# Kernel tuning notes

Measured on AMD Instinct MI355X. Metric: run time of the kernel, lower is better.

## Reference

```python
import jax, jax.numpy as jnp
import numpy as np

EPS = 1e-8
LAM = 20.0  # lambda_softmax
I, R, T, W, D = 128, 48, 64, 100, 768


def l2norm(x, axis=-1):
    # matches torch l2norm: x / (sqrt(sum(x^2)) + eps)
    return x / (jnp.sqrt(jnp.sum(x * x, axis=axis, keepdims=True)) + EPS)


def _safe_div(num, den):
    return num / jnp.where(den > 0, den, 1.0)


def setup_inputs() -> dict:
    key = jax.random.key(0)
    k1, k2, k3, k4, k5 = jax.random.split(key, 5)
    return {
        "local_img_query": jax.random.normal(k1, (I, R, D), jnp.float32),
        "local_img_value": jax.random.normal(k2, (I, R, D), jnp.float32),
        "local_text_key": jax.random.normal(k3, (T, W, D), jnp.float32),
        "local_text_value": jax.random.normal(k4, (T, W, D), jnp.float32),
        "text_length": jax.random.randint(k5, (T,), 8, W + 1),
    }


def reference(local_img_query, local_img_value, local_text_key, local_text_value, text_length):
    # Vectorized over texts: padding words are masked instead of sliced,
    # reproducing the per-text ragged loop of compute_weiTexts exactly.
    Tn, Wn, Dn = local_text_key.shape
    In, Rn, _ = local_img_query.shape
    dtype = local_img_query.dtype
    mask = jnp.arange(Wn)[None, :] < text_length[:, None]          # [T,W] valid words
    Lf = text_length.astype(dtype)

    imgQn = l2norm(local_img_query)                                 # [I,R,D]
    txtKn = l2norm(local_text_key)                                  # [T,W,D]
    # cosine scores, shared by both directions (t2i uses the transpose)
    sim = jnp.einsum('twd,ird->tiwr', txtKn, imgQn)                 # [T,I,W,R]
    a = jax.nn.leaky_relu(sim, 0.1)

    # ---- i2t: query = image regions, source = text words ----
    ai = l2norm(a, axis=-1)                                         # l2norm over R per word row
    ai = jnp.swapaxes(ai, 2, 3)                                     # [T,I,R,W]
    m4 = mask[:, None, None, :]
    attn = jax.nn.softmax(jnp.where(m4, ai * LAM, -1e30), axis=-1)  # softmax over valid words
    attn = attn * m4
    # focal_equal with true source length L_i
    funcF = attn * Lf[:, None, None, None] - jnp.sum(attn, -1, keepdims=True)
    tmp = jnp.where(funcF > 0, attn, 0.0)
    attn = _safe_div(tmp, jnp.sum(tmp, -1, keepdims=True))
    weiText = l2norm(jnp.einsum('tirw,twd->tird', attn, local_text_value))  # [T,I,R,D]
    num = jnp.sum(local_img_value[None] * weiText, -1)
    den = jnp.maximum(jnp.linalg.norm(local_img_value, axis=-1)[None]
                      * jnp.linalg.norm(weiText, axis=-1), EPS)
    i2t = jnp.mean(num / den, axis=-1)                              # [T,I]

    # ---- t2i: query = text words, source = image regions ----
    a2 = jnp.swapaxes(a, 2, 3) * m4                                 # [T,I,R,W]; zero padded words before l2norm over W
    a2 = l2norm(a2, axis=-1)
    a2 = jnp.swapaxes(a2, 2, 3)                                     # [T,I,W,R]
    attn2 = jax.nn.softmax(a2 * LAM, axis=-1)                       # softmax over regions (dense)
    funcF2 = attn2 * Rn - jnp.sum(attn2, -1, keepdims=True)
    tmp2 = jnp.where(funcF2 > 0, attn2, 0.0)
    attn2 = _safe_div(tmp2, jnp.sum(tmp2, -1, keepdims=True))
    weiImage = l2norm(jnp.einsum('tiwr,ird->tiwd', attn2, local_img_value))  # [T,I,W,D]
    num2 = jnp.sum(local_text_value[:, None] * weiImage, -1)        # [T,I,W]
    den2 = jnp.maximum(jnp.linalg.norm(local_text_value, axis=-1)[:, None]
                       * jnp.linalg.norm(weiImage, axis=-1), EPS)
    sim2 = jnp.where(mask[:, None, :], num2 / den2, 0.0)
    t2i = jnp.sum(sim2, axis=-1) / Lf[:, None]                      # masked mean over valid words, [T,I]

    return i2t.T, t2i.T                                             # ([n_img,n_txt], [n_img,n_txt])
```

## Files before the change

### kernel.cpp

```cpp
#include <hip/hip_runtime.h>

#define EPS   1e-8f
#define LAMB  20.0f
#define NI    128
#define NR    48
#define NT    64
#define NW    100
#define ND    768

typedef unsigned int uint;
typedef unsigned short ushortt;
typedef __attribute__((ext_vector_type(8))) short short8;
typedef __attribute__((ext_vector_type(4))) float f32x4;

#define OFF_KHI  102400ULL
#define OFF_KLO  11112448ULL
#define OFF_QHI  22122496ULL
#define OFF_QLO  31559680ULL
#define OFF_TVB  40996864ULL
#define OFF_IVB  52006912ULL
#define OFF_MH   61444096ULL
#define OFF_ML   63279104ULL
#define OFF_HH   65114112ULL
#define OFF_HL   65900544ULL
#define WS_NEED  66686976ULL

__device__ inline unsigned short f2bf(float f) {
    uint u = __float_as_uint(f);
    u = (u + 0x7fffu + ((u >> 16) & 1u)) >> 16;
    return (unsigned short)u;
}
__device__ inline float bf2f(unsigned short h) {
    return __uint_as_float((uint)h << 16);
}
__device__ inline void split_store(float4 v, ushortt* hp, ushortt* lp) {
    unsigned short h0 = f2bf(v.x), h1 = f2bf(v.y), h2 = f2bf(v.z), h3 = f2bf(v.w);
    float f0 = bf2f(h0), f1 = bf2f(h1), f2 = bf2f(h2), f3 = bf2f(h3);
    ushort4 H; H.x = h0; H.y = h1; H.z = h2; H.w = h3;
    ushort4 L2; L2.x = f2bf(v.x - f0); L2.y = f2bf(v.y - f1); L2.z = f2bf(v.z - f2); L2.w = f2bf(v.w - f3);
    *(ushort4*)hp = H;
    *(ushort4*)lp = L2;
}
__device__ inline int swzATT(int r, int w) {
    return r * 128 + ((((w >> 3) ^ (r & 7)) << 3) | (w & 7));
}
__device__ inline int swzATT2(int w, int r) {
    return w * 64 + ((((r >> 3) ^ (w & 7)) << 3) | (r & 7));
}
__device__ inline float wredsum(float v) {
#pragma unroll
    for (int m = 1; m < 64; m <<= 1) v += __shfl_xor(v, m, 64);
    return v;
}
__device__ inline float wredmax(float v) {
#pragma unroll
    for (int m = 1; m < 64; m <<= 1) v = fmaxf(v, __shfl_xor(v, m, 64));
    return v;
}

__global__ void nafs_norms(const float* __restrict__ imgQ,
                           const float* __restrict__ imgV,
                           const float* __restrict__ txtK,
                           const float* __restrict__ txtV,
                           float* __restrict__ ws) {
    int row  = blockIdx.x * 4 + (threadIdx.x >> 6);
    int lane = threadIdx.x & 63;
    const float* src;
    int inv;
    if (row < 6144)       { src = imgQ + (size_t)row * ND;           inv = 1; }
    else if (row < 12544) { src = txtK + (size_t)(row - 6144) * ND;  inv = 1; }
    else if (row < 18688) { src = imgV + (size_t)(row - 12544) * ND; inv = 0; }
    else                  { src = txtV + (size_t)(row - 18688) * ND; inv = 0; }
    float ss = 0.f;
#pragma unroll
    for (int j = 0; j < 3; ++j) {
        float4 v = *(const float4*)(src + j * 256 + lane * 4);
        ss += v.x * v.x + v.y * v.y + v.z * v.z + v.w * v.w;
    }
#pragma unroll
    for (int off = 32; off > 0; off >>= 1) ss += __shfl_down(ss, off, 64);
    if (lane == 0) {
        float n = sqrtf(ss);
        ws[row] = inv ? (1.0f / (n + EPS)) : n;
    }
}

__global__ void nafs_convert(const float* __restrict__ txtK,
                             const float* __restrict__ imgQ,
                             const float* __restrict__ txtV,
                             const float* __restrict__ imgV,
                             const float* __restrict__ ws,
                             ushortt* __restrict__ khi, ushortt* __restrict__ klo,
                             ushortt* __restrict__ qhi, ushortt* __restrict__ qlo,
                             ushortt* __restrict__ tvb, ushortt* __restrict__ ivb) {
    int row = blockIdx.x;
    int c4  = threadIdx.x;
    const int dc32 = c4 >> 3;
    const int quad = (c4 & 7) >> 1;
    const int j0   = (c4 & 1) * 4;
    if (row < 7168) {
        int t = row / 112, w = row % 112;
        int m = w >> 4, l15 = w & 15;
        size_t o = ((size_t)(t * 7 + m) * 24 + dc32) * 512 + (quad * 16 + l15) * 8 + j0;
        if (w < NW) {
            float s = ws[6144 + t * NW + w];
            float4 v = *(const float4*)&txtK[((size_t)t * NW + w) * ND + c4 * 4];
            v.x *= s; v.y *= s; v.z *= s; v.w *= s;
            split_store(v, &khi[o], &klo[o]);
        } else {
            ushort4 z; z.x = z.y = z.z = z.w = 0;
            *(ushort4*)&khi[o] = z; *(ushort4*)&klo[o] = z;
        }
    } else if (row < 13312) {
        int q = row - 7168;
        int ii = q / 48, r = q % 48;
        int n = r >> 4, l15 = r & 15;
        float s = ws[q];
        float4 v = *(const float4*)&imgQ[(size_t)q * ND + c4 * 4];
        v.x *= s; v.y *= s; v.z *= s; v.w *= s;
        size_t o = ((size_t)(ii * 3 + n) * 24 + dc32) * 512 + (quad * 16 + l15) * 8 + j0;
        split_store(v, &qhi[o], &qlo[o]);
    } else if (row < 20480) {
        int rr = row - 13312;
        int t = rr / 112, w = rr % 112;
        int m = w >> 4, l15 = w & 15;
        size_t o = ((size_t)(t * 7 + m) * 24 + dc32) * 512 + (quad * 16 + l15) * 8 + j0;
        ushort4 u; u.x = u.y = u.z = u.w = 0;
        if (w < NW) {
            float4 v = *(const float4*)&txtV[((size_t)t * NW + w) * ND + c4 * 4];
            u.x = f2bf(v.x); u.y = f2bf(v.y); u.z = f2bf(v.z); u.w = f2bf(v.w);
        }
        *(ushort4*)&tvb[o] = u;
    } else {
        int rr = row - 20480;
        int ii = rr / 48, r = rr % 48;
        int n = r >> 4, l15 = r & 15;
        size_t o = ((size_t)(ii * 3 + n) * 24 + dc32) * 512 + (quad * 16 + l15) * 8 + j0;
        float4 v = *(const float4*)&imgV[(size_t)rr * ND + c4 * 4];
        ushort4 u; u.x = f2bf(v.x); u.y = f2bf(v.y); u.z = f2bf(v.z); u.w = f2bf(v.w);
        *(ushort4*)&ivb[o] = u;
    }
}

__global__ void nafs_gram_m(const ushortt* __restrict__ tvb,
                            ushortt* __restrict__ mh, ushortt* __restrict__ ml) {
    const int t = blockIdx.x;
    const int tid = threadIdx.x, wv = tid >> 6, lane = tid & 63;
    const int quad = lane >> 4, l15 = lane & 15;
    const ushortt* base = tvb + (size_t)t * 7 * 24 * 512;
    ushortt* mhB = mh + (size_t)t * 7 * 4 * 512;
    ushortt* mlB = ml + (size_t)t * 7 * 4 * 512;
#pragma unroll
    for (int a = 0; a < 2; ++a) {
        int m = wv + 4 * a;
        if (m < 7) {
            f32x4 c[7];
#pragma unroll
            for (int n = 0; n < 7; ++n) c[n] = (f32x4){0.f, 0.f, 0.f, 0.f};
            for (int dc32 = 0; dc32 < 24; ++dc32) {
                short8 av = *(const short8*)&base[((size_t)m * 24 + dc32) * 512 + lane * 8];
#pragma unroll
                for (int n = 0; n < 7; ++n) {
                    short8 bv = *(const short8*)&base[((size_t)n * 24 + dc32) * 512 + lane * 8];
                    c[n] = __builtin_amdgcn_mfma_f32_16x16x32_bf16(av, bv, c[n], 0, 0, 0);
                }
            }
#pragma unroll
            for (int n = 0; n < 7; ++n)
#pragma unroll
                for (int reg = 0; reg < 4; ++reg) {
                    int wc = n * 16 + l15;
                    int lrow = quad * 4 + reg;
                    float v = c[n][reg];
                    ushortt h = f2bf(v);
                    size_t fo = ((size_t)m * 4 + (wc >> 5)) * 512
                              + ((((wc >> 3) & 3) * 16 + lrow) * 8) + (wc & 7);
                    mhB[fo] = h;
                    mlB[fo] = f2bf(v - bf2f(h));
                }
        }
    }
    for (int idx = tid; idx < 7 * 32; idx += 256) {
        int m = idx >> 5, ln = 32 + (idx & 31);
        short8 z = (short8){0, 0, 0, 0, 0, 0, 0, 0};
        size_t fo = ((size_t)m * 4 + 3) * 512 + (size_t)ln * 8;
        *(short8*)&mhB[fo] = z; *(short8*)&mlB[fo] = z;
    }
}

__global__ void nafs_gram_h(const ushortt* __restrict__ ivb,
                            ushortt* __restrict__ hh, ushortt* __restrict__ hl) {
    const int i = blockIdx.x;
    const int tid = threadIdx.x, wv = tid >> 6, lane = tid & 63;
    const int quad = lane >> 4, l15 = lane & 15;
    const ushortt* base = ivb + (size_t)i * 3 * 24 * 512;
    ushortt* hhB = hh + (size_t)i * 3 * 2 * 512;
    ushortt* hlB = hl + (size_t)i * 3 * 2 * 512;
    if (wv < 3) {
        int m = wv;
        f32x4 c[3];
#pragma unroll
        for (int n = 0; n < 3; ++n) c[n] = (f32x4){0.f, 0.f, 0.f, 0.f};
        for (int dc32 = 0; dc32 < 24; ++dc32) {
            short8 av = *(const short8*)&base[((size_t)m * 24 + dc32) * 512 + lane * 8];
#pragma unroll
            for (int n = 0; n < 3; ++n) {
                short8 bv = *(const short8*)&base[((size_t)n * 24 + dc32) * 512 + lane * 8];
                c[n] = __builtin_amdgcn_mfma_f32_16x16x32_bf16(av, bv, c[n], 0, 0, 0);
            }
        }
#pragma unroll
        for (int n = 0; n < 3; ++n)
#pragma unroll
            for (int reg = 0; reg < 4; ++reg) {
                int rc = n * 16 + l15;
                int lrow = quad * 4 + reg;
                float v = c[n][reg];
                ushortt h = f2bf(v);
                size_t fo = ((size_t)m * 2 + (rc >> 5)) * 512
                          + ((((rc >> 3) & 3) * 16 + lrow) * 8) + (rc & 7);
                hhB[fo] = h;
                hlB[fo] = f2bf(v - bf2f(h));
            }
    }
    for (int idx = tid; idx < 3 * 32; idx += 256) {
        int m = idx >> 5, ln = 32 + (idx & 31);
        short8 z = (short8){0, 0, 0, 0, 0, 0, 0, 0};
        size_t fo = ((size_t)m * 2 + 1) * 512 + (size_t)ln * 8;
        *(short8*)&hhB[fo] = z; *(short8*)&hlB[fo] = z;
    }
}

__global__ __launch_bounds__(256, 2)
void nafs_fused3(const int*  __restrict__ tlen,
                 const float* __restrict__ ws,
                 const ushortt* __restrict__ khi, const ushortt* __restrict__ klo,
                 const ushortt* __restrict__ qhi, const ushortt* __restrict__ qlo,
                 const ushortt* __restrict__ tvb, const ushortt* __restrict__ ivb,
                 const ushortt* __restrict__ mh, const ushortt* __restrict__ ml,
                 const ushortt* __restrict__ hh, const ushortt* __restrict__ hl,
                 float* __restrict__ out) {
    __shared__ __align__(16) ushortt shATT[48 * 128];
    __shared__ __align__(16) ushortt shATT2[112 * 64];
    __shared__ float sCol[NR], sSe1[NR], sS11[NR], sS21[NR];
    __shared__ float sCos1[NR], sCos2[112];
    __shared__ float sSS1[NR], sDD1[NR], sSS2[112], sDD2[112];

    const int tid  = threadIdx.x;
    const int wv   = tid >> 6;
    const int lane = tid & 63;
    const int quad = lane >> 4;
    const int l15  = lane & 15;
    const int key  = l15 & 7;
    const int b    = blockIdx.x;
    const int xcd  = b & 7;
    const int idx  = b >> 3;
    const int st   = idx >> 6;
    const int rem  = idx & 63;
    const int i    = (xcd << 4) | (rem >> 2);
    const int t    = (st << 2) | (rem & 3);
    const int L    = tlen[t];
    const float Lf = (float)L;

    const float* __restrict__ nVi = ws + 12544;
    const float* __restrict__ nVt = ws + 18688;

    if (tid < NR) {
        sSS1[tid] = 0.f; sDD1[tid] = 0.f;
        sCol[tid] = 0.f; sSe1[tid] = 0.f; sS11[tid] = 0.f; sS21[tid] = 0.f;
    }
    for (int idx2 = tid; idx2 < 112 * 2; idx2 += 256) {
        int w = idx2 >> 1, nb = 6 + (idx2 & 1);
        short8 z = (short8){0, 0, 0, 0, 0, 0, 0, 0};
        *(short8*)&shATT2[w * 64 + ((nb ^ (w & 7)) << 3)] = z;
    }
    __syncthreads();

    const int m0  = wv, m1 = wv + 4;
    const int m1c = (m1 == 7) ? 6 : m1;
    const size_t kb0 = ((size_t)(t * 7 + m0)) * 24 * 512 + (size_t)lane * 8;
    const size_t kb1 = ((size_t)(t * 7 + m1c)) * 24 * 512 + (size_t)lane * 8;
    const size_t qb  = ((size_t)(i * 3)) * 24 * 512 + (size_t)lane * 8;
    const ushortt* fK0h = khi + kb0;
    const ushortt* fK0l = klo + kb0;
    const ushortt* fK1h = khi + kb1;
    const ushortt* fK1l = klo + kb1;
    const ushortt* fQh  = qhi + qb;
    const ushortt* fQl  = qlo + qb;
    const ushortt* fA0  = tvb + kb0;
    const ushortt* fA1  = tvb + kb1;
    const ushortt* fB   = ivb + qb;

    f32x4 acc[2][3];
    f32x4 gf[2][3];
#pragma unroll
    for (int a = 0; a < 2; ++a)
#pragma unroll
        for (int n = 0; n < 3; ++n) {
            acc[a][n] = (f32x4){0.f, 0.f, 0.f, 0.f};
            gf[a][n]  = (f32x4){0.f, 0.f, 0.f, 0.f};
        }

    for (int dc32 = 0; dc32 < 24; ++dc32) {
        const int o = dc32 * 512;
        short8 a0h = *(const short8*)(fK0h + o);
        short8 a0l = *(const short8*)(fK0l + o);
        short8 a1h = *(const short8*)(fK1h + o);
        short8 a1l = *(const short8*)(fK1l + o);
        short8 b0h = *(const short8*)(fQh + o);
        short8 b0l = *(const short8*)(fQl + o);
        short8 b1h = *(const short8*)(fQh + 12288 + o);
        short8 b1l = *(const short8*)(fQl + 12288 + o);
        short8 b2h = *(const short8*)(fQh + 24576 + o);
        short8 b2l = *(const short8*)(fQl + 24576 + o);
        short8 tA0 = *(const short8*)(fA0 + o);
        short8 tA1 = *(const short8*)(fA1 + o);
        short8 tB0 = *(const short8*)(fB + o);
        short8 tB1 = *(const short8*)(fB + 12288 + o);
        short8 tB2 = *(const short8*)(fB + 24576 + o);

        acc[0][0] = __builtin_amdgcn_mfma_f32_16x16x32_bf16(a0h, b0h, acc[0][0], 0, 0, 0);
        acc[0][0] = __builtin_amdgcn_mfma_f32_16x16x32_bf16(a0h, b0l, acc[0][0], 0, 0, 0);
        acc[0][0] = __builtin_amdgcn_mfma_f32_16x16x32_bf16(a0l, b0h, acc[0][0], 0, 0, 0);
        acc[0][1] = __builtin_amdgcn_mfma_f32_16x16x32_bf16(a0h, b1h, acc[0][1], 0, 0, 0);
        acc[0][1] = __builtin_amdgcn_mfma_f32_16x16x32_bf16(a0h, b1l, acc[0][1], 0, 0, 0);
        acc[0][1] = __builtin_amdgcn_mfma_f32_16x16x32_bf16(a0l, b1h, acc[0][1], 0, 0, 0);
        acc[0][2] = __builtin_amdgcn_mfma_f32_16x16x32_bf16(a0h, b2h, acc[0][2], 0, 0, 0);
        acc[0][2] = __builtin_amdgcn_mfma_f32_16x16x32_bf16(a0h, b2l, acc[0][2], 0, 0, 0);
        acc[0][2] = __builtin_amdgcn_mfma_f32_16x16x32_bf16(a0l, b2h, acc[0][2], 0, 0, 0);
        acc[1][0] = __builtin_amdgcn_mfma_f32_16x16x32_bf16(a1h, b0h, acc[1][0], 0, 0, 0);
        acc[1][0] = __builtin_amdgcn_mfma_f32_16x16x32_bf16(a1h, b0l, acc[1][0], 0, 0, 0);
        acc[1][0] = __builtin_amdgcn_mfma_f32_16x16x32_bf16(a1l, b0h, acc[1][0], 0, 0, 0);
        acc[1][1] = __builtin_amdgcn_mfma_f32_16x16x32_bf16(a1h, b1h, acc[1][1], 0, 0, 0);
        acc[1][1] = __builtin_amdgcn_mfma_f32_16x16x32_bf16(a1h, b1l, acc[1][1], 0, 0, 0);
        acc[1][1] = __builtin_amdgcn_mfma_f32_16x16x32_bf16(a1l, b1h, acc[1][1], 0, 0, 0);
        acc[1][2] = __builtin_amdgcn_mfma_f32_16x16x32_bf16(a1h, b2h, acc[1][2], 0, 0, 0);
        acc[1][2] = __builtin_amdgcn_mfma_f32_16x16x32_bf16(a1h, b2l, acc[1][2], 0, 0, 0);
        acc[1][2] = __builtin_amdgcn_mfma_f32_16x16x32_bf16(a1l, b2h, acc[1][2], 0, 0, 0);

        gf[0][0] = __builtin_amdgcn_mfma_f32_16x16x32_bf16(tA0, tB0, gf[0][0], 0, 0, 0);
        gf[0][1] = __builtin_amdgcn_mfma_f32_16x16x32_bf16(tA0, tB1, gf[0][1], 0, 0, 0);
        gf[0][2] = __builtin_amdgcn_mfma_f32_16x16x32_bf16(tA0, tB2, gf[0][2], 0, 0, 0);
        gf[1][0] = __builtin_amdgcn_mfma_f32_16x16x32_bf16(tA1, tB0, gf[1][0], 0, 0, 0);
        gf[1][1] = __builtin_amdgcn_mfma_f32_16x16x32_bf16(tA1, tB1, gf[1][1], 0, 0, 0);
        gf[1][2] = __builtin_amdgcn_mfma_f32_16x16x32_bf16(tA1, tB2, gf[1][2], 0, 0, 0);
    }

    float lk[2][3][4];
#pragma unroll
    for (int a = 0; a < 2; ++a) {
        int m = wv + 4 * a;
        bool ok = (m < 7);
#pragma unroll
        for (int n = 0; n < 3; ++n)
#pragma unroll
            for (int reg = 0; reg < 4; ++reg) {
                float s = ok ? acc[a][n][reg] : 0.f;
                lk[a][n][reg] = (s > 0.f) ? s : 0.1f * s;
            }
    }

    float invW[2][4];
#pragma unroll
    for (int a = 0; a < 2; ++a)
#pragma unroll
        for (int reg = 0; reg < 4; ++reg) {
            float ss = 0.f;
#pragma unroll
            for (int n = 0; n < 3; ++n) ss = fmaf(lk[a][n][reg], lk[a][n][reg], ss);
            ss += __shfl_xor(ss, 1, 64); ss += __shfl_xor(ss, 2, 64);
            ss += __shfl_xor(ss, 4, 64); ss += __shfl_xor(ss, 8, 64);
            invW[a][reg] = 1.0f / (sqrtf(ss) + EPS);
        }

    float e1[2][3][4];
    {
        float cs[3] = {0.f, 0.f, 0.f}, es[3] = {0.f, 0.f, 0.f};
#pragma unroll
        for (int a = 0; a < 2; ++a) {
            int m = wv + 4 * a;
#pragma unroll
            for (int reg = 0; reg < 4; ++reg) {
                int w = m * 16 + quad * 4 + reg;
                bool act = (m < 7) && (w < L);
#pragma unroll
                for (int n = 0; n < 3; ++n) {
                    float v = lk[a][n][reg];
                    float e = act ? __expf(v * invW[a][reg] * LAMB) : 0.f;
                    e1[a][n][reg] = e;
                    if (act) cs[n] = fmaf(v, v, cs[n]);
                    es[n] += e;
                }
            }
        }
#pragma unroll
        for (int n = 0; n < 3; ++n) {
            float c = cs[n], e = es[n];
            c += __shfl_xor(c, 16, 64); c += __shfl_xor(c, 32, 64);
            e += __shfl_xor(e, 16, 64); e += __shfl_xor(e, 32, 64);
            if (quad == 0) {
                atomicAdd(&sCol[n * 16 + l15], c);
                atomicAdd(&sSe1[n * 16 + l15], e);
            }
        }
    }
    __syncthreads();

    {
        float inv2[3];
#pragma unroll
        for (int n = 0; n < 3; ++n) inv2[n] = 1.0f / (sqrtf(sCol[n * 16 + l15]) + EPS);
#pragma unroll
        for (int a = 0; a < 2; ++a) {
            int m = wv + 4 * a;
            if (m < 7) {
#pragma unroll
                for (int reg = 0; reg < 4; ++reg) {
                    int w = m * 16 + quad * 4 + reg;
                    float e2[3];
                    float se = 0.f;
#pragma unroll
                    for (int n = 0; n < 3; ++n) {
                        float e = __expf(lk[a][n][reg] * inv2[n] * LAMB);
                        e2[n] = e; se += e;
                    }
                    se += __shfl_xor(se, 1, 64); se += __shfl_xor(se, 2, 64);
                    se += __shfl_xor(se, 4, 64); se += __shfl_xor(se, 8, 64);
                    float inv = 1.0f / se;
                    float S1 = e2[0] * inv + e2[1] * inv + e2[2] * inv;
                    S1 += __shfl_xor(S1, 1, 64); S1 += __shfl_xor(S1, 2, 64);
                    S1 += __shfl_xor(S1, 4, 64); S1 += __shfl_xor(S1, 8, 64);
                    float sel[3];
                    float S2 = 0.f;
#pragma unroll
                    for (int n = 0; n < 3; ++n) {
                        float p = e2[n] * inv;
                        sel[n] = ((p * 48.0f - S1) > 0.f) ? p : 0.f;
                        S2 += sel[n];
                    }
                    S2 += __shfl_xor(S2, 1, 64); S2 += __shfl_xor(S2, 2, 64);
                    S2 += __shfl_xor(S2, 4, 64); S2 += __shfl_xor(S2, 8, 64);
                    float iS2 = 1.0f / ((S2 > 0.f) ? S2 : 1.0f);
                    bool rowOK = (w < L);
#pragma unroll
                    for (int n = 0; n < 3; ++n) {
                        float val = rowOK ? sel[n] * iS2 : 0.f;
                        shATT2[swzATT2(w, n * 16 + l15)] = f2bf(val);
                    }
                }
            }
        }
    }

    float invSe[3];
#pragma unroll
    for (int n = 0; n < 3; ++n) invSe[n] = 1.0f / sSe1[n * 16 + l15];
    {
        float s1p[3] = {0.f, 0.f, 0.f};
#pragma unroll
        for (int a = 0; a < 2; ++a)
#pragma unroll
            for (int n = 0; n < 3; ++n)
#pragma unroll
                for (int reg = 0; reg < 4; ++reg)
                    s1p[n] += e1[a][n][reg] * invSe[n];
#pragma unroll
        for (int n = 0; n < 3; ++n) {
            float v = s1p[n];
            v += __shfl_xor(v, 16, 64); v += __shfl_xor(v, 32, 64);
            if (quad == 0) atomicAdd(&sS11[n * 16 + l15], v);
        }
    }
    __syncthreads();

    {
        float s2p[3] = {0.f, 0.f, 0.f};
#pragma unroll
        for (int n = 0; n < 3; ++n) {
            float S1r = sS11[n * 16 + l15];
#pragma unroll
            for (int a = 0; a < 2; ++a)
#pragma unroll
                for (int reg = 0; reg < 4; ++reg) {
                    float p = e1[a][n][reg] * invSe[n];
                    s2p[n] += ((p * Lf - S1r) > 0.f) ? p : 0.f;
                }
        }
#pragma unroll
        for (int n = 0; n < 3; ++n) {
            float v = s2p[n];
            v += __shfl_xor(v, 16, 64); v += __shfl_xor(v, 32, 64);
            if (quad == 0) atomicAdd(&sS21[n * 16 + l15], v);
        }
    }
    __syncthreads();

    {
#pragma unroll
        for (int n = 0; n < 3; ++n) {
            int r = n * 16 + l15;
            float S1r = sS11[r];
            float s2  = sS21[r];
            float iS2 = 1.0f / ((s2 > 0.f) ? s2 : 1.0f);
#pragma unroll
            for (int a = 0; a < 2; ++a) {
                int m = wv + 4 * a;
                ushortt v4[4];
#pragma unroll
                for (int reg = 0; reg < 4; ++reg) {
                    float p  = e1[a][n][reg] * invSe[n];
                    float tm = ((p * Lf - S1r) > 0.f) ? p : 0.f;
                    v4[reg] = f2bf(tm * iS2);
                }
                int wb = m * 16 + quad * 4;
                int f  = (((wb >> 3) ^ (r & 7)) << 3) | (wb & 7);
                *(ushort4*)&shATT[r * 128 + f] = *(ushort4*)v4;
            }
        }
    }
    __syncthreads();

    {
        float pd1[3] = {0.f, 0.f, 0.f};
#pragma unroll
        for (int a = 0; a < 2; ++a) {
            int m = wv + 4 * a;
            if (m < 7) {
#pragma unroll
                for (int reg = 0; reg < 4; ++reg) {
                    int w = m * 16 + quad * 4 + reg;
                    float p2 = 0.f;
#pragma unroll
                    for (int n = 0; n < 3; ++n) {
                        int r = n * 16 + l15;
                        float gv = gf[a][n][reg];
                        p2 = fmaf(gv, bf2f(shATT2[swzATT2(w, r)]), p2);
                        pd1[n] = fmaf(gv, bf2f(shATT[swzATT(r, w)]), pd1[n]);
                    }
                    p2 += __shfl_xor(p2, 1, 64); p2 += __shfl_xor(p2, 2, 64);
                    p2 += __shfl_xor(p2, 4, 64); p2 += __shfl_xor(p2, 8, 64);
                    if (l15 == 0) sDD2[w] = p2;
                }
            }
        }
#pragma unroll
        for (int n = 0; n < 3; ++n) {
            float p = pd1[n];
            p += __shfl_xor(p, 16, 64); p += __shfl_xor(p, 32, 64);
            if (quad == 0) atomicAdd(&sDD1[n * 16 + l15], p);
        }
    }

    {
        short8 af[3][4];
#pragma unroll
        for (int mt = 0; mt < 3; ++mt)
#pragma unroll
            for (int ks = 0; ks < 4; ++ks)
                af[mt][ks] = *(const short8*)&shATT[(mt * 16 + l15) * 128 + (((ks * 4 + quad) ^ key) << 3)];
        float ps[3][4];
#pragma unroll
        for (int mt = 0; mt < 3; ++mt)
#pragma unroll
            for (int reg = 0; reg < 4; ++reg) ps[mt][reg] = 0.f;
#pragma unroll
        for (int p = 0; p < 2; ++p) {
            int nt = wv + 4 * p;
            if (nt < 7) {
                const ushortt* pMh = mh + ((size_t)(t * 7 + nt)) * 4 * 512 + (size_t)lane * 8;
                const ushortt* pMl = ml + ((size_t)(t * 7 + nt)) * 4 * 512 + (size_t)lane * 8;
                short8 bh[4], bl[4];
#pragma unroll
                for (int ks = 0; ks < 4; ++ks) {
                    bh[ks] = *(const short8*)(pMh + ks * 512);
                    bl[ks] = *(const short8*)(pMl + ks * 512);
                }
                f32x4 y[3];
#pragma unroll
                for (int mt = 0; mt < 3; ++mt) y[mt] = (f32x4){0.f, 0.f, 0.f, 0.f};
#pragma unroll
                for (int mt = 0; mt < 3; ++mt)
#pragma unroll
                    for (int ks = 0; ks < 4; ++ks) {
                        y[mt] = __builtin_amdgcn_mfma_f32_16x16x32_bf16(af[mt][ks], bh[ks], y[mt], 0, 0, 0);
                        y[mt] = __builtin_amdgcn_mfma_f32_16x16x32_bf16(af[mt][ks], bl[ks], y[mt], 0, 0, 0);
                    }
                int wc = nt * 16 + l15;
#pragma unroll
                for (int mt = 0; mt < 3; ++mt)
#pragma unroll
                    for (int reg = 0; reg < 4; ++reg) {
                        int r = mt * 16 + quad * 4 + reg;
                        ps[mt][reg] = fmaf(y[mt][reg], bf2f(shATT[swzATT(r, wc)]), ps[mt][reg]);
                    }
            }
        }
#pragma unroll
        for (int mt = 0; mt < 3; ++mt)
#pragma unroll
            for (int reg = 0; reg < 4; ++reg) {
                float p = ps[mt][reg];
                p += __shfl_xor(p, 1, 64); p += __shfl_xor(p, 2, 64);
                p += __shfl_xor(p, 4, 64); p += __shfl_xor(p, 8, 64);
                if (l15 == 0) atomicAdd(&sSS1[mt * 16 + quad * 4 + reg], p);
            }
    }

    {
        short8 zbh[3][2], zbl[3][2];
#pragma unroll
        for (int n = 0; n < 3; ++n) {
#pragma unroll
            for (int ks = 0; ks < 2; ++ks) {
                size_t fo = (((size_t)(i * 3 + n)) * 2 + ks) * 512 + (size_t)lane * 8;
                zbh[n][ks] = *(const short8*)&hh[fo];
                zbl[n][ks] = *(const short8*)&hl[fo];
            }
        }
#pragma unroll
        for (int a = 0; a < 2; ++a) {
            int m = wv + 4 * a;
            if (m < 7) {
                f32x4 z[3];
#pragma unroll
                for (int n = 0; n < 3; ++n) z[n] = (f32x4){0.f, 0.f, 0.f, 0.f};
#pragma unroll
                for (int ks = 0; ks < 2; ++ks) {
                    short8 a2f = *(const short8*)&shATT2[(m * 16 + l15) * 64 + (((ks * 4 + quad) ^ key) << 3)];
#pragma unroll
                    for (int n = 0; n < 3; ++n) {
                        z[n] = __builtin_amdgcn_mfma_f32_16x16x32_bf16(a2f, zbh[n][ks], z[n], 0, 0, 0);
                        z[n] = __builtin_amdgcn_mfma_f32_16x16x32_bf16(a2f, zbl[n][ks], z[n], 0, 0, 0);
                    }
                }
#pragma unroll
                for (int reg = 0; reg < 4; ++reg) {
                    int w = m * 16 + quad * 4 + reg;
                    float p = 0.f;
#pragma unroll
                    for (int n = 0; n < 3; ++n)
                        p = fmaf(z[n][reg], bf2f(shATT2[swzATT2(w, n * 16 + l15)]), p);
                    p += __shfl_xor(p, 1, 64); p += __shfl_xor(p, 2, 64);
                    p += __shfl_xor(p, 4, 64); p += __shfl_xor(p, 8, 64);
                    if (l15 == 0) sSS2[w] = p;
                }
            }
        }
    }
    __syncthreads();

    if (tid < NR) {
        float s = fmaxf(sSS1[tid], 0.f), d = sDD1[tid];
        float nu  = sqrtf(s);
        float num = d / (nu + EPS);
        float den = fmaxf(nVi[i * NR + tid] * (nu / (nu + EPS)), EPS);
        sCos1[tid] = num / den;
    } else if (tid >= 64 && tid < 176) {
        int w = tid - 64;
        if (w < L) {
            float s = fmaxf(sSS2[w], 0.f), d = sDD2[w];
            float nu  = sqrtf(s);
            float num = d / (nu + EPS);
            float den = fmaxf(nVt[t * NW + w] * (nu / (nu + EPS)), EPS);
            sCos2[w] = num / den;
        }
    }
    __syncthreads();
    if (tid == 0) {
        float s = 0.f;
        for (int r = 0; r < NR; ++r) s += sCos1[r];
        out[i * NT + t] = s * (1.0f / 48.0f);
    } else if (tid == 64) {
        float s = 0.f;
        for (int w = 0; w < L; ++w) s += sCos2[w];
        out[NI * NT + i * NT + t] = s / Lf;
    }
}

#define A_KH   0
#define A_KL   4480
#define A_QH   8960
#define A_QL   10880
#define A_ATT  0
#define A_ATT2 6528
#define SHA_SZ 14592
#define B1_TVT 3200
#define B2_IVT 6656
#define SHB_SZ 4900

__global__ __launch_bounds__(256, 3)
void nafs_fused_fb(const float* __restrict__ imgQ,
                   const float* __restrict__ imgV,
                   const float* __restrict__ txtK,
                   const float* __restrict__ txtV,
                   const int*  __restrict__ tlen,
                   const float* __restrict__ ws,
                   float* __restrict__ out) {
    __shared__ ushortt shA[SHA_SZ];
    __shared__ float shB[SHB_SZ];
    __shared__ float sKs[NW], sQs[NR], sInvW[NW], sInv2[NR], sCos1[NR], sCos2[112];

    const int tid  = threadIdx.x;
    const int wv   = tid >> 6;
    const int lane = tid & 63;
    const int quad = lane >> 4;
    const int l15  = lane & 15;
    const int b    = blockIdx.x;
    const int t    = b >> 7;
    const int i    = b & 127;
    const int L    = tlen[t];
    const float Lf = (float)L;

    const float* __restrict__ invQ = ws;
    const float* __restrict__ invK = ws + 6144;
    const float* __restrict__ nVi  = ws + 12544;
    const float* __restrict__ nVt  = ws + 18688;

    const float* Kbase  = txtK + (size_t)t * (NW * ND);
    const float* Qbase  = imgQ + (size_t)i * (NR * ND);
    const float* TVbase = txtV + (size_t)t * (NW * ND);
    const float* IVbase = imgV + (size_t)i * (NR * ND);

    if (tid < NW)                  sKs[tid]       = invK[t * NW + tid];
    else if (tid < NW + NR)        sQs[tid - NW]  = invQ[i * NR + (tid - NW)];

    const int mt0 = wv * 2, mt1 = wv * 2 + 1;
    f32x4 acc[2][3];
#pragma unroll
    for (int a = 0; a < 2; ++a)
#pragma unroll
        for (int n = 0; n < 3; ++n) acc[a][n] = (f32x4){0.f, 0.f, 0.f, 0.f};

    for (int dc = 0; dc < ND; dc += 32) {
        __syncthreads();
        for (int idx = tid; idx < 112 * 8; idx += 256) {
            int w = idx >> 3, seg = idx & 7;
            float4 v;
            if (w < NW) {
                v = *(const float4*)(Kbase + (size_t)w * ND + dc + seg * 4);
                float s = sKs[w];
                v.x *= s; v.y *= s; v.z *= s; v.w *= s;
            } else { v.x = v.y = v.z = v.w = 0.f; }
            split_store(v, &shA[A_KH + w * 40 + seg * 4], &shA[A_KL + w * 40 + seg * 4]);
        }
        for (int idx = tid; idx < NR * 8; idx += 256) {
            int r = idx >> 3, seg = idx & 7;
            float4 v = *(const float4*)(Qbase + (size_t)r * ND + dc + seg * 4);
            float s = sQs[r];
            v.x *= s; v.y *= s; v.z *= s; v.w *= s;
            split_store(v, &shA[A_QH + r * 40 + seg * 4], &shA[A_QL + r * 40 + seg * 4]);
        }
        __syncthreads();
        short8 bh[3], bl[3];
#pragma unroll
        for (int n = 0; n < 3; ++n) {
            bh[n] = *(const short8*)&shA[A_QH + (n * 16 + l15) * 40 + quad * 8];
            bl[n] = *(const short8*)&shA[A_QL + (n * 16 + l15) * 40 + quad * 8];
        }
#pragma unroll
        for (int a = 0; a < 2; ++a) {
            int m = (a == 0) ? mt0 : mt1;
            if (m < 7) {
                short8 ah = *(const short8*)&shA[A_KH + (m * 16 + l15) * 40 + quad * 8];
                short8 al = *(const short8*)&shA[A_KL + (m * 16 + l15) * 40 + quad * 8];
#pragma unroll
                for (int n = 0; n < 3; ++n) {
                    acc[a][n] = __builtin_amdgcn_mfma_f32_16x16x32_bf16(ah, bh[n], acc[a][n], 0, 0, 0);
                    acc[a][n] = __builtin_amdgcn_mfma_f32_16x16x32_bf16(ah, bl[n], acc[a][n], 0, 0, 0);
                    acc[a][n] = __builtin_amdgcn_mfma_f32_16x16x32_bf16(al, bh[n], acc[a][n], 0, 0, 0);
                }
            }
        }
    }
    __syncthreads();
#pragma unroll
    for (int a = 0; a < 2; ++a) {
        int m = (a == 0) ? mt0 : mt1;
        if (m < 7) {
#pragma unroll
            for (int n = 0; n < 3; ++n)
#pragma unroll
                for (int reg = 0; reg < 4; ++reg) {
                    int w = m * 16 + quad * 4 + reg;
                    if (w < NW) {
                        float s = acc[a][n][reg];
                        shB[w * 49 + n * 16 + l15] = (s > 0.f) ? s : 0.1f * s;
                    }
                }
        }
    }
    __syncthreads();

    if (tid < NW) {
        float ssum = 0.f;
#pragma unroll 8
        for (int r = 0; r < NR; ++r) { float v = shB[tid * 49 + r]; ssum += v * v; }
        sInvW[tid] = 1.0f / (sqrtf(ssum) + EPS);
    } else if (tid >= 128 && tid < 128 + NR) {
        int r = tid - 128;
        float ssum = 0.f;
        for (int w = 0; w < L; ++w) { float v = shB[w * 49 + r]; ssum += v * v; }
        sInv2[r] = 1.0f / (sqrtf(ssum) + EPS);
    }
    __syncthreads();

    for (int r = wv; r < NR; r += 4) {
        int w1 = lane, w2 = lane + 64;
        int v1ok = (w1 < L), v2ok = (w2 < L);
        float v1 = v1ok ? shB[w1 * 49 + r] * sInvW[w1] * LAMB : -1e30f;
        float v2 = v2ok ? shB[w2 * 49 + r] * sInvW[w2] * LAMB : -1e30f;
        float m  = wredmax(fmaxf(v1, v2));
        float e1 = v1ok ? expf(v1 - m) : 0.f;
        float e2 = v2ok ? expf(v2 - m) : 0.f;
        float inv = 1.0f / wredsum(e1 + e2);
        float p1 = e1 * inv, p2 = e2 * inv;
        float S1 = wredsum(p1 + p2);
        float t1 = ((p1 * Lf - S1) > 0.f) ? p1 : 0.f;
        float t2 = ((p2 * Lf - S1) > 0.f) ? p2 : 0.f;
        float S2 = wredsum(t1 + t2);
        float iS2 = 1.0f / ((S2 > 0.f) ? S2 : 1.0f);
        shA[A_ATT + r * 136 + w1] = f2bf(t1 * iS2);
        shA[A_ATT + r * 136 + w2] = f2bf(t2 * iS2);
    }
    for (int w = wv; w < L; w += 4) {
        int rok = (lane < NR);
        float v = rok ? shB[w * 49 + lane] * sInv2[lane] * LAMB : -1e30f;
        float m = wredmax(v);
        float e = rok ? expf(v - m) : 0.f;
        float inv = 1.0f / wredsum(e);
        float p = e * inv;
        float S1 = wredsum(p);
        float tm = ((p * 48.0f - S1) > 0.f) ? p : 0.f;
        float S2 = wredsum(tm);
        float iS2 = 1.0f / ((S2 > 0.f) ? S2 : 1.0f);
        shA[A_ATT2 + w * 72 + lane] = f2bf(tm * iS2);
    }
    for (int w = L + wv; w < 112; w += 4) shA[A_ATT2 + w * 72 + lane] = 0;
    __syncthreads();

    ushortt* shBu = (ushortt*)shB;
    const int kk = (L + 31) >> 5;
    float ss1[4] = {0.f, 0.f, 0.f, 0.f}, dd1[4] = {0.f, 0.f, 0.f, 0.f};
    const int mt = wv;
    const int cgrp = tid >> 5, ccol = tid & 31;

    for (int cc = 0; cc < ND; cc += 32) {
        __syncthreads();
        for (int w = cgrp; w < 128; w += 8) {
            float val = (w < NW) ? TVbase[(size_t)w * ND + cc + ccol] : 0.f;
            shBu[B1_TVT + ccol * 136 + w] = f2bf(val);
        }
        for (int idx = tid; idx < NR * 8; idx += 256) {
            int r = idx >> 3, seg = idx & 7;
            float4 v = *(const float4*)(IVbase + (size_t)r * ND + cc + seg * 4);
            float* p = &shB[r * 33 + seg * 4];
            p[0] = v.x; p[1] = v.y; p[2] = v.z; p[3] = v.w;
        }
        __syncthreads();
        if (mt < 3) {
            f32x4 u[2] = {(f32x4){0.f,0.f,0.f,0.f}, (f32x4){0.f,0.f,0.f,0.f}};
            for (int ks = 0; ks < kk; ++ks) {
                short8 a = *(const short8*)&shA[A_ATT + (mt * 16 + l15) * 136 + ks * 32 + quad * 8];
#pragma unroll
                for (int n = 0; n < 2; ++n) {
                    short8 bb = *(const short8*)&shBu[B1_TVT + (n * 16 + l15) * 136 + ks * 32 + quad * 8];
                    u[n] = __builtin_amdgcn_mfma_f32_16x16x32_bf16(a, bb, u[n], 0, 0, 0);
                }
            }
#pragma unroll
            for (int n = 0; n < 2; ++n)
#pragma unroll
                for (int reg = 0; reg < 4; ++reg) {
                    int r = mt * 16 + quad * 4 + reg;
                    float uu = u[n][reg];
                    ss1[reg] = fmaf(uu, uu, ss1[reg]);
                    dd1[reg] = fmaf(uu, shB[r * 33 + n * 16 + l15], dd1[reg]);
                }
        }
    }
    if (mt < 3) {
#pragma unroll
        for (int reg = 0; reg < 4; ++reg) {
            float s = ss1[reg], d = dd1[reg];
#pragma unroll
            for (int m = 1; m < 16; m <<= 1) { s += __shfl_xor(s, m, 64); d += __shfl_xor(d, m, 64); }
            if (l15 == 0) {
                int r = mt * 16 + quad * 4 + reg;
                float nu  = sqrtf(s);
                float num = d / (nu + EPS);
                float den = fmaxf(nVi[i * NR + r] * (nu / (nu + EPS)), EPS);
                sCos1[r] = num / den;
            }
        }
    }

    const int ntot = (L + 15) >> 4;
    float ss2[2] = {0.f, 0.f}, dd2[2] = {0.f, 0.f};

    for (int cc = 0; cc < ND; cc += 32) {
        __syncthreads();
        for (int idx = tid; idx < NW * 8; idx += 256) {
            int w = idx >> 3, seg = idx & 7;
            float4 v = *(const float4*)(TVbase + (size_t)w * ND + cc + seg * 4);
            float* p = &shB[w * 33 + seg * 4];
            p[0] = v.x; p[1] = v.y; p[2] = v.z; p[3] = v.w;
        }
        for (int r = cgrp; r < 64; r += 8) {
            float val = (r < NR) ? IVbase[(size_t)r * ND + cc + ccol] : 0.f;
            shBu[B2_IVT + ccol * 72 + r] = f2bf(val);
        }
        __syncthreads();
#pragma unroll
        for (int pp = 0; pp < 2; ++pp) {
            int nt = wv + 4 * pp;
            if (nt < ntot) {
                f32x4 u[2] = {(f32x4){0.f,0.f,0.f,0.f}, (f32x4){0.f,0.f,0.f,0.f}};
#pragma unroll
                for (int ks = 0; ks < 2; ++ks) {
                    short8 bb = *(const short8*)&shA[A_ATT2 + (nt * 16 + l15) * 72 + ks * 32 + quad * 8];
#pragma unroll
                    for (int mm = 0; mm < 2; ++mm) {
                        short8 aa = *(const short8*)&shBu[B2_IVT + (mm * 16 + l15) * 72 + ks * 32 + quad * 8];
                        u[mm] = __builtin_amdgcn_mfma_f32_16x16x32_bf16(aa, bb, u[mm], 0, 0, 0);
                    }
                }
                int w = nt * 16 + l15;
                float tvok = (w < L) ? 1.f : 0.f;
#pragma unroll
                for (int mm = 0; mm < 2; ++mm)
#pragma unroll
                    for (int reg = 0; reg < 4; ++reg) {
                        int c = mm * 16 + quad * 4 + reg;
                        float uu = u[mm][reg];
                        float tv = (w < L) ? shB[w * 33 + c] : 0.f;
                        ss2[pp] = fmaf(uu, uu, ss2[pp]);
                        dd2[pp] = fmaf(uu, tv * tvok, dd2[pp]);
                    }
            }
        }
    }
#pragma unroll
    for (int pp = 0; pp < 2; ++pp) {
        int nt = wv + 4 * pp;
        if (nt < ntot) {
            float s = ss2[pp], d = dd2[pp];
            s += __shfl_xor(s, 16, 64); d += __shfl_xor(d, 16, 64);
            s += __shfl_xor(s, 32, 64); d += __shfl_xor(d, 32, 64);
            if (quad == 0) {
                int w = nt * 16 + l15;
                if (w < L) {
                    float nu  = sqrtf(s);
                    float num = d / (nu + EPS);
                    float den = fmaxf(nVt[t * NW + w] * (nu / (nu + EPS)), EPS);
                    sCos2[w] = num / den;
                }
            }
        }
    }
    __syncthreads();
    if (tid == 0) {
        float s = 0.f;
        for (int r = 0; r < NR; ++r) s += sCos1[r];
        out[i * NT + t] = s * (1.0f / 48.0f);
    } else if (tid == 64) {
        float s = 0.f;
        for (int w = 0; w < L; ++w) s += sCos2[w];
        out[NI * NT + i * NT + t] = s / Lf;
    }
}

extern "C" void kernel_launch(void* const* d_in, const int* in_sizes, int n_in,
                              void* d_out, int out_size, void* d_ws, size_t ws_size,
                              hipStream_t stream) {
    (void)in_sizes; (void)n_in; (void)out_size;
    const float* imgQ = (const float*)d_in[0];
    const float* imgV = (const float*)d_in[1];
    const float* txtK = (const float*)d_in[2];
    const float* txtV = (const float*)d_in[3];
    const int*   tlen = (const int*)d_in[4];
    float* ws  = (float*)d_ws;
    float* out = (float*)d_out;

    hipLaunchKernelGGL(nafs_norms, dim3(6272), dim3(256), 0, stream,
                       imgQ, imgV, txtK, txtV, ws);

    if (ws_size >= WS_NEED) {
        char* base = (char*)d_ws;
        ushortt* khi = (ushortt*)(base + OFF_KHI);
        ushortt* klo = (ushortt*)(base + OFF_KLO);
        ushortt* qhi = (ushortt*)(base + OFF_QHI);
        ushortt* qlo = (ushortt*)(base + OFF_QLO);
        ushortt* tvb = (ushortt*)(base + OFF_TVB);
        ushortt* ivb = (ushortt*)(base + OFF_IVB);
        ushortt* mh  = (ushortt*)(base + OFF_MH);
        ushortt* ml  = (ushortt*)(base + OFF_ML);
        ushortt* hh  = (ushortt*)(base + OFF_HH);
        ushortt* hl  = (ushortt*)(base + OFF_HL);
        hipLaunchKernelGGL(nafs_convert, dim3(26624), dim3(192), 0, stream,
                           txtK, imgQ, txtV, imgV, ws, khi, klo, qhi, qlo, tvb, ivb);
        hipLaunchKernelGGL(nafs_gram_m, dim3(64), dim3(256), 0, stream, tvb, mh, ml);
        hipLaunchKernelGGL(nafs_gram_h, dim3(128), dim3(256), 0, stream, ivb, hh, hl);
        hipLaunchKernelGGL(nafs_fused3, dim3(NT * NI), dim3(256), 0, stream,
                           tlen, ws, khi, klo, qhi, qlo, tvb, ivb, mh, ml, hh, hl, out);
    } else {
        hipLaunchKernelGGL(nafs_fused_fb, dim3(NT * NI), dim3(256), 0, stream,
                           imgQ, imgV, txtK, txtV, tlen, ws, out);
    }
}
```

Baseline: 661.7 us.

## Stage image-query fragments through double-buffered LDS and prefetch next chunk

Each wave used to load all nine image-side fragments (Q hi/lo and image values) from global memory on its own, so every block fetched them four times. Now the four waves split those loads, write them into a double-buffered shared-memory tile, and read them back for the MFMAs. The text-side fragments and the next chunk's image fragments are loaded one iteration ahead in registers. This cuts redundant global traffic and hides load latency, at the cost of a __syncthreads per chunk, more LDS, and extra register pressure under launch_bounds(256,2).

```diff
diff --git a/kernel.cpp b/kernel.cpp
--- a/kernel.cpp
+++ b/kernel.cpp
@@ -242,6 +242,7 @@
                  float* __restrict__ out) {
     __shared__ __align__(16) ushortt shATT[48 * 128];
     __shared__ __align__(16) ushortt shATT2[112 * 64];
+    __shared__ __align__(16) ushortt shQ[2 * 9 * 512];
     __shared__ float sCol[NR], sSe1[NR], sS11[NR], sS21[NR];
     __shared__ float sCos1[NR], sCos2[112];
     __shared__ float sSS1[NR], sDD1[NR], sSS2[112], sDD2[112];
@@ -274,7 +275,6 @@
         short8 z = (short8){0, 0, 0, 0, 0, 0, 0, 0};
         *(short8*)&shATT2[w * 64 + ((nb ^ (w & 7)) << 3)] = z;
     }
-    __syncthreads();
 
     const int m0  = wv, m1 = wv + 4;
     const int m1c = (m1 == 7) ? 6 : m1;
@@ -301,49 +301,94 @@
             gf[a][n]  = (f32x4){0.f, 0.f, 0.f, 0.f};
         }
 
+    short8 c0h = *(const short8*)(fK0h);
+    short8 c0l = *(const short8*)(fK0l);
+    short8 c1h = *(const short8*)(fK1h);
+    short8 c1l = *(const short8*)(fK1l);
+    short8 ct0 = *(const short8*)(fA0);
+    short8 ct1 = *(const short8*)(fA1);
+    {
+        ushortt* dst = shQ + lane * 8;
+        if (wv == 0) {
+            *(short8*)(dst + 0 * 512) = *(const short8*)(fQh);
+            *(short8*)(dst + 4 * 512) = *(const short8*)(fQh + 24576);
+            *(short8*)(dst + 8 * 512) = *(const short8*)(fB + 24576);
+        } else if (wv == 1) {
+            *(short8*)(dst + 1 * 512) = *(const short8*)(fQl);
+            *(short8*)(dst + 5 * 512) = *(const short8*)(fQl + 24576);
+        } else if (wv == 2) {
+            *(short8*)(dst + 2 * 512) = *(const short8*)(fQh + 12288);
+            *(short8*)(dst + 6 * 512) = *(const short8*)(fB);
+        } else {
+            *(short8*)(dst + 3 * 512) = *(const short8*)(fQl + 12288);
+            *(short8*)(dst + 7 * 512) = *(const short8*)(fB + 12288);
+        }
+    }
+    __syncthreads();
+
     for (int dc32 = 0; dc32 < 24; ++dc32) {
-        const int o = dc32 * 512;
-        short8 a0h = *(const short8*)(fK0h + o);
-        short8 a0l = *(const short8*)(fK0l + o);
-        short8 a1h = *(const short8*)(fK1h + o);
-        short8 a1l = *(const short8*)(fK1l + o);
-        short8 b0h = *(const short8*)(fQh + o);
-        short8 b0l = *(const short8*)(fQl + o);
-        short8 b1h = *(const short8*)(fQh + 12288 + o);
-        short8 b1l = *(const short8*)(fQl + 12288 + o);
-        short8 b2h = *(const short8*)(fQh + 24576 + o);
-        short8 b2l = *(const short8*)(fQl + 24576 + o);
-        short8 tA0 = *(const short8*)(fA0 + o);
-        short8 tA1 = *(const short8*)(fA1 + o);
-        short8 tB0 = *(const short8*)(fB + o);
-        short8 tB1 = *(const short8*)(fB + 12288 + o);
-        short8 tB2 = *(const short8*)(fB + 24576 + o);
-
-        acc[0][0] = __builtin_amdgcn_mfma_f32_16x16x32_bf16(a0h, b0h, acc[0][0], 0, 0, 0);
-        acc[0][0] = __builtin_amdgcn_mfma_f32_16x16x32_bf16(a0h, b0l, acc[0][0], 0, 0, 0);
-        acc[0][0] = __builtin_amdgcn_mfma_f32_16x16x32_bf16(a0l, b0h, acc[0][0], 0, 0, 0);
-        acc[0][1] = __builtin_amdgcn_mfma_f32_16x16x32_bf16(a0h, b1h, acc[0][1], 0, 0, 0);
-        acc[0][1] = __builtin_amdgcn_mfma_f32_16x16x32_bf16(a0h, b1l, acc[0][1], 0, 0, 0);
-        acc[0][1] = __builtin_amdgcn_mfma_f32_16x16x32_bf16(a0l, b1h, acc[0][1], 0, 0, 0);
-        acc[0][2] = __builtin_amdgcn_mfma_f32_16x16x32_bf16(a0h, b2h, acc[0][2], 0, 0, 0);
-        acc[0][2] = __builtin_amdgcn_mfma_f32_16x16x32_bf16(a0h, b2l, acc[0][2], 0, 0, 0);
-        acc[0][2] = __builtin_amdgcn_mfma_f32_16x16x32_bf16(a0l, b2h, acc[0][2], 0, 0, 0);
-        acc[1][0] = __builtin_amdgcn_mfma_f32_16x16x32_bf16(a1h, b0h, acc[1][0], 0, 0, 0);
-        acc[1][0] = __builtin_amdgcn_mfma_f32_16x16x32_bf16(a1h, b0l, acc[1][0], 0, 0, 0);
-        acc[1][0] = __builtin_amdgcn_mfma_f32_16x16x32_bf16(a1l, b0h, acc[1][0], 0, 0, 0);
-        acc[1][1] = __builtin_amdgcn_mfma_f32_16x16x32_bf16(a1h, b1h, acc[1][1], 0, 0, 0);
-        acc[1][1] = __builtin_amdgcn_mfma_f32_16x16x32_bf16(a1h, b1l, acc[1][1], 0, 0, 0);
-        acc[1][1] = __builtin_amdgcn_mfma_f32_16x16x32_bf16(a1l, b1h, acc[1][1], 0, 0, 0);
-        acc[1][2] = __builtin_amdgcn_mfma_f32_16x16x32_bf16(a1h, b2h, acc[1][2], 0, 0, 0);
-        acc[1][2] = __builtin_amdgcn_mfma_f32_16x16x32_bf16(a1h, b2l, acc[1][2], 0, 0, 0);
-        acc[1][2] = __builtin_amdgcn_mfma_f32_16x16x32_bf16(a1l, b2h, acc[1][2], 0, 0, 0);
-
-        gf[0][0] = __builtin_amdgcn_mfma_f32_16x16x32_bf16(tA0, tB0, gf[0][0], 0, 0, 0);
-        gf[0][1] = __builtin_amdgcn_mfma_f32_16x16x32_bf16(tA0, tB1, gf[0][1], 0, 0, 0);
-        gf[0][2] = __builtin_amdgcn_mfma_f32_16x16x32_bf16(tA0, tB2, gf[0][2], 0, 0, 0);
-        gf[1][0] = __builtin_amdgcn_mfma_f32_16x16x32_bf16(tA1, tB0, gf[1][0], 0, 0, 0);
-        gf[1][1] = __builtin_amdgcn_mfma_f32_16x16x32_bf16(tA1, tB1, gf[1][1], 0, 0, 0);
-        gf[1][2] = __builtin_amdgcn_mfma_f32_16x16x32_bf16(tA1, tB2, gf[1][2], 0, 0, 0);
+        const int bb = dc32 & 1;
+        short8 n0h, n0l, n1h, n1l, nt0, nt1;
+        short8 s0, s1, s2;
+        if (dc32 < 23) {
+            const int o = (dc32 + 1) * 512;
+            n0h = *(const short8*)(fK0h + o);
+            n0l = *(const short8*)(fK0l + o);
+            n1h = *(const short8*)(fK1h + o);
+            n1l = *(const short8*)(fK1l + o);
+            nt0 = *(const short8*)(fA0 + o);
+            nt1 = *(const short8*)(fA1 + o);
+            if (wv == 0) {
+                s0 = *(const short8*)(fQh + o);
+                s1 = *(const short8*)(fQh + 24576 + o);
+                s2 = *(const short8*)(fB + 24576 + o);
+            } else if (wv == 1) {
+                s0 = *(const short8*)(fQl + o);
+                s1 = *(const short8*)(fQl + 24576 + o);
+            } else if (wv == 2) {
+                s0 = *(const short8*)(fQh + 12288 + o);
+                s1 = *(const short8*)(fB + o);
+            } else {
+                s0 = *(const short8*)(fQl + 12288 + o);
+                s1 = *(const short8*)(fB + 12288 + o);
+            }
+        }
+        {
+            const ushortt* qs = shQ + bb * (9 * 512) + lane * 8;
+#pragma unroll
+            for (int n = 0; n < 3; ++n) {
+                short8 bh = *(const short8*)(qs + (2 * n) * 512);
+                short8 bl = *(const short8*)(qs + (2 * n + 1) * 512);
+                short8 tB = *(const short8*)(qs + (6 + n) * 512);
+                acc[0][n] = __builtin_amdgcn_mfma_f32_16x16x32_bf16(c0h, bh, acc[0][n], 0, 0, 0);
+                acc[0][n] = __builtin_amdgcn_mfma_f32_16x16x32_bf16(c0h, bl, acc[0][n], 0, 0, 0);
+                acc[0][n] = __builtin_amdgcn_mfma_f32_16x16x32_bf16(c0l, bh, acc[0][n], 0, 0, 0);
+                acc[1][n] = __builtin_amdgcn_mfma_f32_16x16x32_bf16(c1h, bh, acc[1][n], 0, 0, 0);
+                acc[1][n] = __builtin_amdgcn_mfma_f32_16x16x32_bf16(c1h, bl, acc[1][n], 0, 0, 0);
+                acc[1][n] = __builtin_amdgcn_mfma_f32_16x16x32_bf16(c1l, bh, acc[1][n], 0, 0, 0);
+                gf[0][n]  = __builtin_amdgcn_mfma_f32_16x16x32_bf16(ct0, tB, gf[0][n], 0, 0, 0);
+                gf[1][n]  = __builtin_amdgcn_mfma_f32_16x16x32_bf16(ct1, tB, gf[1][n], 0, 0, 0);
+            }
+        }
+        if (dc32 < 23) {
+            ushortt* dst = shQ + (bb ^ 1) * (9 * 512) + lane * 8;
+            if (wv == 0) {
+                *(short8*)(dst + 0 * 512) = s0;
+                *(short8*)(dst + 4 * 512) = s1;
+                *(short8*)(dst + 8 * 512) = s2;
+            } else if (wv == 1) {
+                *(short8*)(dst + 1 * 512) = s0;
+                *(short8*)(dst + 5 * 512) = s1;
+            } else if (wv == 2) {
+                *(short8*)(dst + 2 * 512) = s0;
+                *(short8*)(dst + 6 * 512) = s1;
+            } else {
+                *(short8*)(dst + 3 * 512) = s0;
+                *(short8*)(dst + 7 * 512) = s1;
+            }
+            c0h = n0h; c0l = n0l; c1h = n1h; c1l = n1l; ct0 = nt0; ct1 = nt1;
+        }
+        __syncthreads();
     }
 
     float lk[2][3][4];
```

New measurement: 646.3 us. 2.3% less time.
